# Optimization experiments

Hardware: AMD Instinct MI355X
Metric: run time of the kernel (lower is better)

Reference implementation:

```python
import jax, jax.numpy as jnp
import numpy as np

B, S, DIM = 2, 4096, 1024
H, HD = 16, 64          # num_heads, head_dim (DIM = H*HD)
KN = 64                 # k neighbors per query
SCALE = 1.0 / np.sqrt(HD)
CANTOR_DEPTH = 8


def _cantor_coords(seq_len: int, depth: int = CANTOR_DEPTH) -> np.ndarray:
    """Vectorized replica of CantorAttention._compute_cantor_coord."""
    x = np.arange(seq_len, dtype=np.float64) / max(1, seq_len - 1)
    x = np.clip(x, 1e-06, 1.0 - 1e-06)
    val = np.zeros(seq_len, dtype=np.float64)
    factor = 0.5
    for _ in range(depth):
        xs = x * 3.0
        digit = np.floor(xs)
        x = xs - digit
        val += factor * (digit == 2)
        factor *= 0.5
    return val.astype(np.float32)


def _build_routes(seq_len: int, k: int) -> np.ndarray:
    coords = _cantor_coords(seq_len)
    dist = np.abs(coords[:, None] - coords[None, :])  # [S, S]
    routes = np.argsort(dist, axis=1, kind='stable')[:, :k]  # k smallest
    return routes.astype(np.int32)


def setup_inputs() -> dict:
    key = jax.random.key(0)
    kx, kw1, kb1, kw2, kb2 = jax.random.split(key, 5)
    x = jax.random.normal(kx, (B, S, DIM), dtype=jnp.float32)
    # learned params (qkv and out projections)
    W_qkv = jax.random.normal(kw1, (DIM, 3 * DIM), dtype=jnp.float32) * (1.0 / np.sqrt(DIM))
    b_qkv = jax.random.normal(kb1, (3 * DIM,), dtype=jnp.float32) * 0.01
    W_out = jax.random.normal(kw2, (DIM, DIM), dtype=jnp.float32) * (1.0 / np.sqrt(DIM))
    b_out = jax.random.normal(kb2, (DIM,), dtype=jnp.float32) * 0.01
    routes = jnp.asarray(_build_routes(S, KN))  # [S, KN] int32, positional Cantor kNN
    return {"x": x, "W_qkv": W_qkv, "b_qkv": b_qkv, "W_out": W_out, "b_out": b_out, "routes": routes}


def reference(x, W_qkv, b_qkv, W_out, b_out, routes):
    Bs, Sl, _ = x.shape
    qkv = x @ W_qkv + b_qkv                                   # [B,S,3*DIM]
    qkv = qkv.reshape(Bs, Sl, 3, H, HD).transpose(2, 0, 3, 1, 4)
    q, k, v = qkv[0], qkv[1], qkv[2]                          # [B,H,S,HD]
    k_g = k[:, :, routes, :]                                  # [B,H,S,KN,HD]
    v_g = v[:, :, routes, :]                                  # [B,H,S,KN,HD]
    scores = jnp.einsum('bhqd,bhqkd->bhqk', q, k_g) * SCALE   # [B,H,S,KN]
    attn = jax.nn.softmax(scores, axis=-1)
    out = jnp.einsum('bhqk,bhqkd->bhqd', attn, v_g)           # [B,H,S,HD]
    out = out.transpose(0, 2, 1, 3).reshape(Bs, Sl, DIM)
    return out @ W_out + b_out
```

## Files before the change

kernel.cpp:

```cpp
#include <hip/hip_runtime.h>
#include <hip/hip_bf16.h>
#include <stdint.h>

#define DEVI __device__ __forceinline__

typedef __bf16 bf16x8 __attribute__((ext_vector_type(8)));
typedef float f32x4 __attribute__((ext_vector_type(4)));
typedef unsigned short ushort8v __attribute__((ext_vector_type(8)));

static constexpr int SEQ = 4096;
static constexpr int DIM_ = 1024;
static constexpr int NH = 16;
static constexpr int HD_ = 64;
static constexpr float SCALE_ = 0.125f;

DEVI unsigned short f2bf(float f) {
  __hip_bfloat16 h = __float2bfloat16(f);
  return __builtin_bit_cast(unsigned short, h);
}


__global__ void k_cvt_bf16(const float* __restrict__ in, unsigned short* __restrict__ out) {
  int i = (blockIdx.x * 256 + threadIdx.x) * 4;
  float4 v = *reinterpret_cast<const float4*>(in + i);
  ushort4 o;
  o.x = f2bf(v.x); o.y = f2bf(v.y); o.z = f2bf(v.z); o.w = f2bf(v.w);
  *reinterpret_cast<ushort4*>(out + i) = o;
}

__global__ void k_transpose_cvt(const float* __restrict__ in, unsigned short* __restrict__ out,
                                int K, int N) {
  __shared__ float tile[64][65];
  const int n0 = blockIdx.x * 64, k0 = blockIdx.y * 64;
  const int tr = threadIdx.x >> 6, tc = threadIdx.x & 63;
#pragma unroll
  for (int p = 0; p < 16; ++p) {
    int r = p * 4 + tr;
    tile[r][tc] = in[(size_t)(k0 + r) * N + n0 + tc];
  }
  __syncthreads();
#pragma unroll
  for (int p = 0; p < 16; ++p) {
    int r = p * 4 + tr;
    out[(size_t)(n0 + r) * K + k0 + tc] = f2bf(tile[tc][r]);
  }
}


DEVI void load16_lds(const void* g, void* l) {
  __builtin_amdgcn_global_load_lds((__attribute__((address_space(1))) void*)(g),
                                   (__attribute__((address_space(3))) void*)(l),
                                   16, 0, 0);
}

template <int MODE>
__global__ __launch_bounds__(256, 4)
void k_gemm_bt(const unsigned short* __restrict__ A,
               const unsigned short* __restrict__ Bt,
               const float* __restrict__ bias,
               float* __restrict__ outF,
               unsigned short* __restrict__ outQ,
               unsigned short* __restrict__ outK,
               unsigned short* __restrict__ outV,
               int M, int N, int K) {
  constexpr int BK = 32;
  __shared__ alignas(16) unsigned short As[2][128 * BK];
  __shared__ alignas(16) unsigned short Bs[2][128 * BK];
  const int tid = threadIdx.x;
  const int wave = tid >> 6, lane = tid & 63;
  const int wr = wave >> 1, wc = wave & 1;
  const int l15 = lane & 15, q = lane >> 4;
  const int bm = blockIdx.x * 128, bn = blockIdx.y * 128;

  f32x4 acc[4][4] = {};

  const int srow = lane >> 2;
  const int scol = ((lane & 3) ^ ((lane >> 3) & 3)) * 8;
  const unsigned short* aS0 = A + (size_t)(bm + wave * 16 + srow) * K + scol;
  const unsigned short* aS1 = aS0 + (size_t)64 * K;
  const unsigned short* bS0 = Bt + (size_t)(bn + wave * 16 + srow) * K + scol;
  const unsigned short* bS1 = bS0 + (size_t)64 * K;
  const int dOff = (wave * 16) * BK;

  const int x3 = (l15 >> 1) & 3;
  const int aRdOff = (wr * 64 + l15) * BK + (q ^ x3) * 8;
  const int bRdOff = (wc * 64 + l15) * BK + (q ^ x3) * 8;

  load16_lds(aS0, &As[0][dOff]);
  load16_lds(aS1, &As[0][dOff + 64 * BK]);
  load16_lds(bS0, &Bs[0][dOff]);
  load16_lds(bS1, &Bs[0][dOff + 64 * BK]);
  __syncthreads();

  const int NT = K / BK;
#pragma unroll 1
  for (int t = 0; t < NT; ++t) {
    const int cur = t & 1;
    if (t + 1 < NT) {
      const int k1 = (t + 1) * BK;
      const int nxt = cur ^ 1;
      load16_lds(aS0 + k1, &As[nxt][dOff]);
      load16_lds(aS1 + k1, &As[nxt][dOff + 64 * BK]);
      load16_lds(bS0 + k1, &Bs[nxt][dOff]);
      load16_lds(bS1 + k1, &Bs[nxt][dOff + 64 * BK]);
    }

    bf16x8 af[4], bfr[4];
#pragma unroll
    for (int m = 0; m < 4; ++m)
      af[m] = *reinterpret_cast<const bf16x8*>(&As[cur][aRdOff + m * 16 * BK]);
#pragma unroll
    for (int n = 0; n < 4; ++n)
      bfr[n] = *reinterpret_cast<const bf16x8*>(&Bs[cur][bRdOff + n * 16 * BK]);
#pragma unroll
    for (int m = 0; m < 4; ++m)
#pragma unroll
      for (int n = 0; n < 4; ++n)
        acc[m][n] = __builtin_amdgcn_mfma_f32_16x16x32_bf16(af[m], bfr[n], acc[m][n], 0, 0, 0);

    __syncthreads();
  }

  const int r0 = q * 4;
#pragma unroll
  for (int m = 0; m < 4; ++m) {
#pragma unroll
    for (int n = 0; n < 4; ++n) {
      const int col = bn + wc * 64 + n * 16 + l15;
      const float bv = bias[col];
#pragma unroll
      for (int j = 0; j < 4; ++j) {
        const int row = bm + wr * 64 + m * 16 + r0 + j;
        const float v = acc[m][n][j] + bv;
        if constexpr (MODE == 0) {
          outF[(size_t)row * N + col] = v;
        } else {
          const int t = col >> 10;
          const int hh = (col >> 6) & 15;
          const int d = col & 63;
          const int b = row >> 12;
          const int s = row & 4095;
          unsigned short* dst = (t == 0) ? outQ : (t == 1) ? outK : outV;
          dst[((size_t)(b * NH + hh) * SEQ + s) * HD_ + d] = f2bf(v);
        }
      }
    }
  }
}


__global__ void k_init(int* __restrict__ tileQ, int* __restrict__ cnt,
                       int* __restrict__ pos, int* __restrict__ nTiles) {
  const int i = blockIdx.x * 256 + threadIdx.x;
  tileQ[i] = -1;
  if (i < 4096) { cnt[i] = 0; pos[i] = 0; }
  if (i == 0) *nTiles = 0;
}

__global__ void k_gid(const int* __restrict__ routes, int* __restrict__ gid, int* __restrict__ cnt) {
  const int s = blockIdx.x * 256 + threadIdx.x;
  const int lead = routes[s * 64];
  int g = s;
  if (lead >= 0 && lead < SEQ && lead != s) {
    bool eq = true;
    const int4* a = reinterpret_cast<const int4*>(routes + (size_t)s * 64);
    const int4* b = reinterpret_cast<const int4*>(routes + (size_t)lead * 64);
#pragma unroll
    for (int i = 0; i < 16; ++i) {
      int4 x = a[i], y = b[i];
      eq = eq && (x.x == y.x) && (x.y == y.y) && (x.z == y.z) && (x.w == y.w);
    }
    if (eq) g = lead;
  }
  gid[s] = g;
  atomicAdd(&cnt[g], 1);
}

__global__ void k_tilebase(const int* __restrict__ cnt, int* __restrict__ tileBase,
                           int* __restrict__ nTiles) {
  const int g = blockIdx.x * 256 + threadIdx.x;
  const int c = cnt[g];
  if (c > 0) {
    tileBase[g] = atomicAdd(nTiles, (c + 15) >> 4);
  }
}

__global__ void k_scatter(const int* __restrict__ gid, const int* __restrict__ tileBase,
                          int* __restrict__ pos, int* __restrict__ tileQ,
                          int* __restrict__ tileLead) {
  const int s = blockIdx.x * 256 + threadIdx.x;
  const int g = gid[s];
  const int p = atomicAdd(&pos[g], 1);
  const int tile = tileBase[g] + (p >> 4);
  tileQ[tile * 16 + (p & 15)] = s;
  if ((p & 15) == 0) tileLead[tile] = g;
}


__global__ __launch_bounds__(256)
void k_attn_grp(const unsigned short* __restrict__ Q,
                const unsigned short* __restrict__ Kb,
                const unsigned short* __restrict__ Vb,
                const int* __restrict__ routes,
                const int* __restrict__ tileQ,
                const int* __restrict__ tileLead,
                const int* __restrict__ nTilesPtr,
                unsigned short* __restrict__ att) {
  const int nT = *nTilesPtr;

  __shared__ int sMemRaw[16];
  __shared__ int sMemEff[16];
  __shared__ int sRoutes[64];
  __shared__ alignas(16) unsigned short sK[4][4096];
  __shared__ alignas(16) unsigned short sV[4][4096];
  __shared__ alignas(16) unsigned short sP[4][16 * 72];

  const int tid = threadIdx.x;
  const int wave = tid >> 6, lane = tid & 63;
  unsigned short* KL = sK[wave];
  unsigned short* VL = sV[wave];
  unsigned short* P = sP[wave];
  const int hi = lane >> 4;
  const int l15 = lane & 15;
  const int l7 = lane & 7;
  const int rr = lane >> 3;

  const int bh = blockIdx.x * 4 + wave;
  const size_t base = (size_t)bh * (SEQ * HD_);
  const int b = bh >> 4, h = bh & 15;

  for (int tile = blockIdx.y; tile < nT; tile += gridDim.y) {
    __syncthreads();
    if (tid < 16) {
      const int v = tileQ[tile * 16 + tid];
      const int v0 = tileQ[tile * 16];
      sMemRaw[tid] = v;
      sMemEff[tid] = (v < 0) ? v0 : v;
    } else if (tid >= 64 && tid < 128) {
      const int lead = tileLead[tile];
      sRoutes[tid - 64] = routes[(size_t)lead * 64 + (tid - 64)];
    }
    __syncthreads();

    bf16x8 qa0, qa1;
    {
      const unsigned short* qrow = Q + base + (size_t)sMemEff[l15] * HD_ + hi * 8;
      qa0 = *reinterpret_cast<const bf16x8*>(qrow);
      qa1 = *reinterpret_cast<const bf16x8*>(qrow + 32);
    }

    {
      const int sc = ((l7 - rr) & 7) * 8;
#pragma unroll
      for (int t = 0; t < 8; ++t) {
        const int rk = sRoutes[t * 8 + rr];
        load16_lds(Kb + base + (size_t)rk * HD_ + sc, &KL[t * 512]);
      }
    }
    {
#pragma unroll
      for (int t = 0; t < 8; ++t) {
        const int rk = sRoutes[t * 8 + rr];
        const int sc = ((l7 - 2 * (t & 3)) & 7) * 8;
        load16_lds(Vb + base + (size_t)rk * HD_ + sc, &VL[t * 512]);
      }
    }

    asm volatile("s_waitcnt vmcnt(8)" ::: "memory");
    __builtin_amdgcn_sched_barrier(0);

    f32x4 accS[4] = {};
    __builtin_amdgcn_s_setprio(1);
#pragma unroll
    for (int nb = 0; nb < 4; ++nb) {
      const int key = nb * 16 + l15;
      const int rot = 8 * (key & 7);
      const int ae0 = key * 64 + (((hi * 8) + rot) & 63);
      const int ae1 = key * 64 + (((32 + hi * 8) + rot) & 63);
      bf16x8 kf0 = *reinterpret_cast<const bf16x8*>(&KL[ae0]);
      bf16x8 kf1 = *reinterpret_cast<const bf16x8*>(&KL[ae1]);
      accS[nb] = __builtin_amdgcn_mfma_f32_16x16x32_bf16(qa0, kf0, accS[nb], 0, 0, 0);
      accS[nb] = __builtin_amdgcn_mfma_f32_16x16x32_bf16(qa1, kf1, accS[nb], 0, 0, 0);
    }
    __builtin_amdgcn_s_setprio(0);

#pragma unroll
    for (int jj = 0; jj < 4; ++jj) {
      float m = fmaxf(fmaxf(accS[0][jj], accS[1][jj]), fmaxf(accS[2][jj], accS[3][jj]));
#pragma unroll
      for (int o = 1; o < 16; o <<= 1) m = fmaxf(m, __shfl_xor(m, o));
      const float e0 = __expf((accS[0][jj] - m) * SCALE_);
      const float e1 = __expf((accS[1][jj] - m) * SCALE_);
      const float e2 = __expf((accS[2][jj] - m) * SCALE_);
      const float e3 = __expf((accS[3][jj] - m) * SCALE_);
      float sum = (e0 + e1) + (e2 + e3);
#pragma unroll
      for (int o = 1; o < 16; o <<= 1) sum += __shfl_xor(sum, o);
      const float rs = __builtin_amdgcn_rcpf(sum);
      const int row = hi * 4 + jj;
      P[row * 72 + 0 + l15] = f2bf(e0 * rs);
      P[row * 72 + 16 + l15] = f2bf(e1 * rs);
      P[row * 72 + 32 + l15] = f2bf(e2 * rs);
      P[row * 72 + 48 + l15] = f2bf(e3 * rs);
    }

    asm volatile("s_waitcnt vmcnt(0) lgkmcnt(0)" ::: "memory");
    __builtin_amdgcn_sched_barrier(0);

    f32x4 accO[4] = {};
#pragma unroll
    for (int ks = 0; ks < 2; ++ks) {
      bf16x8 pf = *reinterpret_cast<const bf16x8*>(&P[l15 * 72 + ks * 32 + hi * 8]);
#pragma unroll
      for (int nb = 0; nb < 4; ++nb) {
        const int d = nb * 16 + l15;
        const int rot = (d + 16 * hi) & 63;
        bf16x8 vf;
#pragma unroll
        for (int j = 0; j < 8; ++j) {
          const int k = ks * 32 + hi * 8 + j;
          vf[j] = *reinterpret_cast<const __bf16*>(&VL[k * 64 + rot]);
        }
        __builtin_amdgcn_s_setprio(1);
        accO[nb] = __builtin_amdgcn_mfma_f32_16x16x32_bf16(pf, vf, accO[nb], 0, 0, 0);
        __builtin_amdgcn_s_setprio(0);
      }
    }

#pragma unroll
    for (int jj = 0; jj < 4; ++jj) {
      const int sQ = sMemRaw[hi * 4 + jj];
      if (sQ >= 0) {
#pragma unroll
        for (int nb = 0; nb < 4; ++nb) {
          att[((size_t)(b * SEQ + sQ)) * DIM_ + h * HD_ + nb * 16 + l15] = f2bf(accO[nb][jj]);
        }
      }
    }
  }
}


extern "C" void kernel_launch(void* const* d_in, const int* in_sizes, int n_in,
                              void* d_out, int out_size, void* d_ws, size_t ws_size,
                              hipStream_t stream) {
  (void)in_sizes; (void)n_in; (void)out_size; (void)ws_size;
  const float* x      = (const float*)d_in[0];
  const float* Wqkv   = (const float*)d_in[1];
  const float* bqkv   = (const float*)d_in[2];
  const float* Wout   = (const float*)d_in[3];
  const float* bout   = (const float*)d_in[4];
  const int*   routes = (const int*)d_in[5];
  float* out = (float*)d_out;

  uint8_t* ws = (uint8_t*)d_ws;
  unsigned short* wqkvT = (unsigned short*)(ws);
  unsigned short* woutT = (unsigned short*)(ws + 6291456);
  unsigned short* Qb    = (unsigned short*)(ws + 8388608);
  unsigned short* Kb    = (unsigned short*)(ws + 25165824);
  unsigned short* Vb    = (unsigned short*)(ws + 41943040);
  unsigned short* att   = (unsigned short*)(ws + 58720256);

  unsigned short* xb = (unsigned short*)d_out;
  uint8_t* g0 = (uint8_t*)d_out + (16u << 20);
  int* gidArr   = (int*)(g0);
  int* cnt      = (int*)(g0 + 16384);
  int* pos      = (int*)(g0 + 32768);
  int* tileBase = (int*)(g0 + 49152);
  int* nTiles   = (int*)(g0 + 65536);
  int* tileLead = (int*)(g0 + 81920);
  int* tileQ    = (int*)(g0 + 98304);

  k_init<<<256, 256, 0, stream>>>(tileQ, cnt, pos, nTiles);
  k_gid<<<16, 256, 0, stream>>>(routes, gidArr, cnt);
  k_tilebase<<<16, 256, 0, stream>>>(cnt, tileBase, nTiles);
  k_scatter<<<16, 256, 0, stream>>>(gidArr, tileBase, pos, tileQ, tileLead);

  k_cvt_bf16<<<8192, 256, 0, stream>>>(x, xb);
  k_transpose_cvt<<<dim3(48, 16), 256, 0, stream>>>(Wqkv, wqkvT, 1024, 3072);
  k_transpose_cvt<<<dim3(16, 16), 256, 0, stream>>>(Wout, woutT, 1024, 1024);

  k_gemm_bt<1><<<dim3(64, 24), 256, 0, stream>>>(xb, wqkvT, bqkv, nullptr, Qb, Kb, Vb,
                                                 8192, 3072, 1024);
  k_attn_grp<<<dim3(8, 64), 256, 0, stream>>>(Qb, Kb, Vb, routes, tileQ, tileLead,
                                              nTiles, att);
  k_gemm_bt<0><<<dim3(64, 8), 256, 0, stream>>>(att, woutT, bout, out,
                                                nullptr, nullptr, nullptr, 8192, 1024, 1024);
}
```

Before: 157.5 us.

## Load B fragments directly to registers, stage only A in LDS with BK=64

```diff
diff --git a/kernel.cpp b/kernel.cpp
--- a/kernel.cpp
+++ b/kernel.cpp
@@ -54,7 +54,7 @@
 }
 
 template <int MODE>
-__global__ __launch_bounds__(256, 4)
+__global__ __launch_bounds__(256, 2)
 void k_gemm_bt(const unsigned short* __restrict__ A,
                const unsigned short* __restrict__ Bt,
                const float* __restrict__ bias,
@@ -63,63 +63,83 @@
                unsigned short* __restrict__ outK,
                unsigned short* __restrict__ outV,
                int M, int N, int K) {
-  constexpr int BK = 32;
+  constexpr int BK = 64;
   __shared__ alignas(16) unsigned short As[2][128 * BK];
-  __shared__ alignas(16) unsigned short Bs[2][128 * BK];
   const int tid = threadIdx.x;
   const int wave = tid >> 6, lane = tid & 63;
   const int wr = wave >> 1, wc = wave & 1;
   const int l15 = lane & 15, q = lane >> 4;
   const int bm = blockIdx.x * 128, bn = blockIdx.y * 128;
+  const int NT = K >> 6;
 
   f32x4 acc[4][4] = {};
 
-  const int srow = lane >> 2;
-  const int scol = ((lane & 3) ^ ((lane >> 3) & 3)) * 8;
-  const unsigned short* aS0 = A + (size_t)(bm + wave * 16 + srow) * K + scol;
-  const unsigned short* aS1 = aS0 + (size_t)64 * K;
-  const unsigned short* bS0 = Bt + (size_t)(bn + wave * 16 + srow) * K + scol;
-  const unsigned short* bS1 = bS0 + (size_t)64 * K;
-  const int dOff = (wave * 16) * BK;
-
-  const int x3 = (l15 >> 1) & 3;
-  const int aRdOff = (wr * 64 + l15) * BK + (q ^ x3) * 8;
-  const int bRdOff = (wc * 64 + l15) * BK + (q ^ x3) * 8;
-
-  load16_lds(aS0, &As[0][dOff]);
-  load16_lds(aS1, &As[0][dOff + 64 * BK]);
-  load16_lds(bS0, &Bs[0][dOff]);
-  load16_lds(bS1, &Bs[0][dOff + 64 * BK]);
-  __syncthreads();
-
-  const int NT = K / BK;
+  const int srow0 = wave * 32 + (lane >> 3);
+  const int srow1 = srow0 + 8;
+  const int ca0 = (lane & 7) ^ ((srow0 >> 1) & 7);
+  const int ca1 = (lane & 7) ^ ((srow1 >> 1) & 7);
+  const unsigned short* aP0 = A + (size_t)(bm + srow0) * K + ca0 * 8;
+  const unsigned short* aP1 = A + (size_t)(bm + srow1) * K + ca1 * 8;
+  const size_t K16 = (size_t)16 * K;
+
+#define STAGEA(T, BUF)                                                  \
+  {                                                                     \
+    const int kk = (T) * 64;                                            \
+    load16_lds(aP0 + kk, &As[BUF][(wave * 32 + 0) * 64]);               \
+    load16_lds(aP1 + kk, &As[BUF][(wave * 32 + 8) * 64]);               \
+    load16_lds(aP0 + K16 + kk, &As[BUF][(wave * 32 + 16) * 64]);        \
+    load16_lds(aP1 + K16 + kk, &As[BUF][(wave * 32 + 24) * 64]);        \
+  }
+
+  const unsigned short* bGB = Bt + (size_t)(bn + wc * 64 + l15) * K + q * 8;
+
+#define LOADB(BANK, T)                                                  \
+  {                                                                     \
+    const int kk = (T) * 64;                                            \
+    _Pragma("unroll") for (int n = 0; n < 4; ++n) {                     \
+      BANK[0][n] = *reinterpret_cast<const bf16x8*>(bGB + (size_t)n * K16 + kk);      \
+      BANK[1][n] = *reinterpret_cast<const bf16x8*>(bGB + (size_t)n * K16 + kk + 32); \
+    }                                                                   \
+  }
+
+  const int x7 = (l15 >> 1) & 7;
+
+#define TILE_BODY(T, BUF, BCUR)                                          \
+  {                                                                      \
+    const int tn = ((T) + 1 < NT) ? (T) + 1 : NT - 1;                    \
+    const int tb = ((T) + 2 < NT) ? (T) + 2 : NT - 1;                    \
+    STAGEA(tn, BUF ^ 1);                                                 \
+    _Pragma("unroll") for (int ks = 0; ks < 2; ++ks) {                   \
+      bf16x8 af[4];                                                      \
+      _Pragma("unroll") for (int m = 0; m < 4; ++m)                      \
+        af[m] = *reinterpret_cast<const bf16x8*>(                        \
+            &As[BUF][(wr * 64 + m * 16 + l15) * 64 + ((ks * 4 + q) ^ x7) * 8]); \
+      _Pragma("unroll") for (int m = 0; m < 4; ++m)                      \
+        _Pragma("unroll") for (int n = 0; n < 4; ++n)                    \
+          acc[m][n] = __builtin_amdgcn_mfma_f32_16x16x32_bf16(           \
+              af[m], BCUR[ks][n], acc[m][n], 0, 0, 0);                   \
+    }                                                                    \
+    asm volatile("s_waitcnt vmcnt(4)" ::: "memory");                     \
+    LOADB(BCUR, tb);                                                     \
+    asm volatile("s_waitcnt vmcnt(8)" ::: "memory");                     \
+    __builtin_amdgcn_s_barrier();                                        \
+  }
+
+  bf16x8 bA[2][4], bB[2][4];
+  LOADB(bA, 0);
+  STAGEA(0, 0);
+  LOADB(bB, 1);
+  asm volatile("s_waitcnt vmcnt(8)" ::: "memory");
+  __builtin_amdgcn_s_barrier();
+
 #pragma unroll 1
-  for (int t = 0; t < NT; ++t) {
-    const int cur = t & 1;
-    if (t + 1 < NT) {
-      const int k1 = (t + 1) * BK;
-      const int nxt = cur ^ 1;
-      load16_lds(aS0 + k1, &As[nxt][dOff]);
-      load16_lds(aS1 + k1, &As[nxt][dOff + 64 * BK]);
-      load16_lds(bS0 + k1, &Bs[nxt][dOff]);
-      load16_lds(bS1 + k1, &Bs[nxt][dOff + 64 * BK]);
-    }
-
-    bf16x8 af[4], bfr[4];
-#pragma unroll
-    for (int m = 0; m < 4; ++m)
-      af[m] = *reinterpret_cast<const bf16x8*>(&As[cur][aRdOff + m * 16 * BK]);
-#pragma unroll
-    for (int n = 0; n < 4; ++n)
-      bfr[n] = *reinterpret_cast<const bf16x8*>(&Bs[cur][bRdOff + n * 16 * BK]);
-#pragma unroll
-    for (int m = 0; m < 4; ++m)
-#pragma unroll
-      for (int n = 0; n < 4; ++n)
-        acc[m][n] = __builtin_amdgcn_mfma_f32_16x16x32_bf16(af[m], bfr[n], acc[m][n], 0, 0, 0);
-
-    __syncthreads();
-  }
+  for (int t = 0; t < NT; t += 2) {
+    TILE_BODY(t, 0, bA);
+    TILE_BODY(t + 1, 1, bB);
+  }
+#undef TILE_BODY
+#undef LOADB
+#undef STAGEA
 
   const int r0 = q * 4;
 #pragma unroll
```

Result: slower. 227.8 us (+44.6%).
